# Performance work log

Hardware: AMD Instinct MI355X
Metric: run time of the kernel (lower is better)

## Reference

```python
import jax, jax.numpy as jnp
import numpy as np

S, B, D, T, E, H = 8, 32, 5, 30, 768, 128


def _time_lstm(Wall, ball, Uall, bU, Wd, bd, x, ts):
    # x: [N,T,E], ts: [N,T]. Faithful to torch TimeLSTM: c_tmp uses sigmoid,
    # and the returned per-step 'outputs' are the o-gates (as in the source).
    N = x.shape[0]
    h0 = jnp.zeros((N, Wd.shape[0]), x.dtype)

    def step(carry, inp):
        h, c = carry
        xt, tt = inp
        c_s1 = jnp.tanh(c @ Wd + bd)
        c_adj = c - c_s1 + c_s1 * tt[:, None]
        g = jax.nn.sigmoid(h @ Wall + ball + xt @ Uall + bU)
        f, i, o, ct = jnp.split(g, 4, axis=1)
        c2 = f * c_adj + i * ct
        h2 = o * jnp.tanh(c2)
        return (h2, c2), o

    _, outs = jax.lax.scan(step, (h0, h0), (x.swapaxes(0, 1), ts.swapaxes(0, 1)))
    return outs.swapaxes(0, 1)  # [N,T,H]


def _attn(W1, b1, W2, b2, V, bV, full, last, lens):
    # full: [N,T,H]; last: [N,H] or [N,1,H]
    s1 = last @ W1 + b1
    if s1.ndim == 2:
        s1 = s1[:, None, :]
    score = jnp.tanh(s1 + full @ W2 + b2) @ V + bV  # [N,T,1]
    if lens is not None:
        mask = jnp.arange(full.shape[1])[None, :] < lens[:, None]
        score = jnp.where(mask[..., None], score, -jnp.inf)
    w = jax.nn.softmax(score, axis=1)
    return jnp.sum(w * full, axis=1)  # [N,H]


def _lstm(Wih, bih, Whh, bhh, x):
    # standard torch LSTM gate order i,f,g,o; x: [N,D,H]
    N = x.shape[0]
    Hh = Whh.shape[0]
    h0 = jnp.zeros((N, Hh), x.dtype)

    def step(carry, xt):
        h, c = carry
        g = xt @ Wih + bih + h @ Whh + bhh
        i, f, gg, o = jnp.split(g, 4, axis=1)
        c2 = jax.nn.sigmoid(f) * c + jax.nn.sigmoid(i) * jnp.tanh(gg)
        h2 = jax.nn.sigmoid(o) * jnp.tanh(c2)
        return (h2, c2), h2

    (h, c), hs = jax.lax.scan(step, (h0, h0), x.swapaxes(0, 1))
    return hs.swapaxes(0, 1), h  # [N,D,H], [N,H]


def _per_stock(tl_Wall, tl_ball, tl_Uall, tl_bU, tl_Wd, tl_bd,
               a1_W1, a1_b1, a1_W2, a1_b2, a1_V, a1_bV,
               l2_Wih, l2_bih, l2_Whh, l2_bhh,
               a2_W1, a2_b1, a2_W2, a2_b2, a2_V, a2_bV,
               x1_W, x1_b, x2_W, x2_b, sent, lens, times):
    # sent: [B,D,T,E], lens: [B,D] int, times: [B,D,T]
    b, d, t, e = sent.shape
    x = sent.reshape(b * d, t, e)
    ts = times.reshape(b * d, t)
    ln = lens.reshape(b * d)
    outs = _time_lstm(tl_Wall, tl_ball, tl_Uall, tl_bU, tl_Wd, tl_bd, x, ts)
    idx = jnp.clip(ln - 1, 0, t - 1)
    hn = outs[jnp.arange(b * d), idx]
    hn = jnp.where((ln > 0)[:, None], hn, 0.0)
    ctx = _attn(a1_W1, a1_b1, a1_W2, a1_b2, a1_V, a1_bV, outs, hn, ln)  # [B*D,H]
    seq = ctx.reshape(b, d, -1)
    hs, hlast = _lstm(l2_Wih, l2_bih, l2_Whh, l2_bhh, seq)
    ctx2 = _attn(a2_W1, a2_b1, a2_W2, a2_b2, a2_V, a2_bV, hs, hlast[:, None, :], None)
    y = jax.nn.relu(ctx2 @ x1_W + x1_b)  # dropout is eval-mode identity
    return y @ x2_W + x2_b  # [B,64]


def setup_inputs() -> dict:
    key = jax.random.key(0)
    ks = iter(jax.random.split(key, 64))

    def p(*shape):
        return jax.random.normal(next(ks), shape, jnp.float32) * 0.05

    H4 = 4 * H
    return {
        'stock_feats': jax.random.normal(next(ks), (B, 2 * S + 1), jnp.float32),
        'sentence_feat': jax.random.normal(next(ks), (B, S, D, T, E), jnp.float32),
        'time_feats': jax.random.uniform(next(ks), (B, S, D, T), jnp.float32),
        'len_tweets': jax.random.randint(next(ks), (B, S, D), 1, T + 1),
        'tl_Wall': p(S, H, H4), 'tl_ball': p(S, H4),
        'tl_Uall': p(S, E, H4), 'tl_bU': p(S, H4),
        'tl_Wd': p(S, H, H), 'tl_bd': p(S, H),
        'a1_W1': p(S, H, H), 'a1_b1': p(S, H), 'a1_W2': p(S, H, H), 'a1_b2': p(S, H),
        'a1_V': p(S, H, 1), 'a1_bV': p(S, 1),
        'l2_Wih': p(S, H, H4), 'l2_bih': p(S, H4), 'l2_Whh': p(S, H, H4), 'l2_bhh': p(S, H4),
        'a2_W1': p(S, H, H), 'a2_b1': p(S, H), 'a2_W2': p(S, H, H), 'a2_b2': p(S, H),
        'a2_V': p(S, H, 1), 'a2_bV': p(S, 1),
        'x1_W': p(S, H, H), 'x1_b': p(S, H), 'x2_W': p(S, H, 64), 'x2_b': p(S, 64),
        'h1_W': p(2 * S + 1, 64), 'h1_b': p(64),
        'h2_W': p(64, 32), 'h2_b': p(32),
        'hc_W': p(64 * S + 32, S), 'hc_b': p(S),
    }


def reference(stock_feats, sentence_feat, time_feats, len_tweets,
              tl_Wall, tl_ball, tl_Uall, tl_bU, tl_Wd, tl_bd,
              a1_W1, a1_b1, a1_W2, a1_b2, a1_V, a1_bV,
              l2_Wih, l2_bih, l2_Whh, l2_bhh,
              a2_W1, a2_b1, a2_W2, a2_b2, a2_V, a2_bV,
              x1_W, x1_b, x2_W, x2_b,
              h1_W, h1_b, h2_W, h2_b, hc_W, hc_b):
    sent = sentence_feat.transpose(1, 0, 2, 3, 4)  # [S,B,D,T,E]
    lens = len_tweets.transpose(1, 0, 2)           # [S,B,D]
    times = time_feats.transpose(1, 0, 2, 3)       # [S,B,D,T]
    per = jax.vmap(_per_stock)(
        tl_Wall, tl_ball, tl_Uall, tl_bU, tl_Wd, tl_bd,
        a1_W1, a1_b1, a1_W2, a1_b2, a1_V, a1_bV,
        l2_Wih, l2_bih, l2_Whh, l2_bhh,
        a2_W1, a2_b1, a2_W2, a2_b2, a2_V, a2_bV,
        x1_W, x1_b, x2_W, x2_b, sent, lens, times)  # [S,B,64]
    text = per.transpose(1, 0, 2).reshape(sent.shape[1], -1)  # [B, S*64]
    xs = jax.nn.relu(stock_feats @ h1_W + h1_b) @ h2_W + h2_b  # [B,32]
    full = jnp.concatenate([xs, text], axis=1)
    return jnp.tanh(full @ hc_W + hc_b)  # [B,S]
```

## Files before the change

kernel.cpp:

```cpp
#include <hip/hip_runtime.h>
#include <cstddef>


typedef __attribute__((ext_vector_type(8))) _Float16 f16x8;
typedef __attribute__((ext_vector_type(4))) _Float16 f16x4;
typedef __attribute__((ext_vector_type(2))) _Float16 f16x2;
typedef __attribute__((ext_vector_type(4))) float f32x4;

__device__ __forceinline__ float rcp_(float x) { return __builtin_amdgcn_rcpf(x); }
__device__ __forceinline__ float sigf(float x) { return rcp_(1.0f + __expf(-x)); }
__device__ __forceinline__ float tanhf_(float x) { return 1.0f - 2.0f * rcp_(__expf(2.0f * x) + 1.0f); }

__device__ __forceinline__ void barrier_lds_only() {
  asm volatile("s_waitcnt lgkmcnt(0)" ::: "memory");
  __builtin_amdgcn_s_barrier();
  __builtin_amdgcn_sched_barrier(0);
}

__global__ __launch_bounds__(256) void k0_rowmap(const int* __restrict__ lens,
                                                 int* __restrict__ rowmap,
                                                 int* __restrict__ Ms) {
  const int s = blockIdx.x;
  const int tid = threadIdx.x;
  __shared__ int st[160];
  __shared__ int ln[160];
  if (tid < 160) {
    const int b = tid / 5, d = tid % 5;
    ln[tid] = lens[(b * 8 + s) * 5 + d];
  }
  __syncthreads();
  if (tid == 0) {
    int run = 0;
    for (int n = 0; n < 160; ++n) { st[n] = run; run += ln[n]; }
    Ms[s] = run;
  }
  __syncthreads();
  if (tid < 160) {
    const int base = st[tid], l = ln[tid];
    for (int t = 0; t < l; ++t) rowmap[s * 4800 + base + t] = tid * 30 + t;
  }
}

__global__ __launch_bounds__(256) void k0_usplit(const float* __restrict__ U,
                                                 _Float16* __restrict__ Uh) {
  const int s = blockIdx.z;
  const int k0 = blockIdx.x * 64;
  const int n0 = blockIdx.y * 64;
  const int tid = threadIdx.x;
  __shared__ _Float16 Th[64 * 66];
  const float* Us = U + (size_t)s * 768 * 512;
#pragma unroll
  for (int rep = 0; rep < 16; ++rep) {
    const int idx = rep * 256 + tid;
    const int r = idx >> 6, c = idx & 63;
    Th[r * 66 + c] = (_Float16)Us[(size_t)(k0 + r) * 512 + n0 + c];
  }
  __syncthreads();
  _Float16* uhs = Uh + (size_t)s * 512 * 768;
#pragma unroll
  for (int rep = 0; rep < 8; ++rep) {
    const int idx = rep * 256 + tid;
    const int nn = idx >> 5;
    const int kp = (idx & 31) * 2;
    const f16x2 h2 = {Th[kp * 66 + nn], Th[(kp + 1) * 66 + nn]};
    *(f16x2*)&uhs[(size_t)(n0 + nn) * 768 + k0 + kp] = h2;
  }
}

__global__ __launch_bounds__(256) void k0_wprep(const float* __restrict__ Wall,
                                                const float* __restrict__ Wd,
                                                _Float16* __restrict__ Wfh,
                                                _Float16* __restrict__ Dfh) {
  const int w = blockIdx.x, s = blockIdx.y;
  const int tid = threadIdx.x;
  const float* Ws = Wall + (size_t)s * 65536;
  _Float16* oh = Wfh + (size_t)(s * 8 + w) * 8192;
  for (int c = tid; c < 1024; c += 256) {
    const int kt = c >> 8, nt = (c >> 6) & 3, l = c & 63;
    const int n = nt * 128 + w * 16 + (l & 15);
    const int kb = kt * 32 + ((l >> 4) << 3);
    f16x8 hv;
#pragma unroll
    for (int e = 0; e < 8; ++e) hv[e] = (_Float16)Ws[(size_t)(kb + e) * 512 + n];
    *(f16x8*)&oh[c * 8] = hv;
  }
  {
    const float* Ds = Wd + (size_t)s * 16384;
    _Float16* od = Dfh + (size_t)(s * 8 + w) * 2048;
    const int c = tid;
    const int kt = c >> 6, l = c & 63;
    const int n = w * 16 + (l & 15);
    const int kb = kt * 32 + ((l >> 4) << 3);
    f16x8 hv;
#pragma unroll
    for (int e = 0; e < 8; ++e) hv[e] = (_Float16)Ds[(size_t)(kb + e) * 128 + n];
    *(f16x8*)&od[c * 8] = hv;
  }
}

__global__ __launch_bounds__(256) void k0_aprep(const float* __restrict__ W1,
                                                const float* __restrict__ W2,
                                                _Float16* __restrict__ W1f,
                                                _Float16* __restrict__ W2f) {
  const int w = blockIdx.x, s = blockIdx.y;
  const int c = threadIdx.x;
  const int kt = c >> 6, l = c & 63;
  const int n = w * 16 + (l & 15);
  const int kb = kt * 32 + ((l >> 4) << 3);
  const float* W1s = W1 + (size_t)s * 16384;
  const float* W2s = W2 + (size_t)s * 16384;
  f16x8 v1, v2;
#pragma unroll
  for (int e = 0; e < 8; ++e) {
    v1[e] = (_Float16)W1s[(size_t)(kb + e) * 128 + n];
    v2[e] = (_Float16)W2s[(size_t)(kb + e) * 128 + n];
  }
  *(f16x8*)&W1f[(size_t)(s * 8 + w) * 2048 + c * 8] = v1;
  *(f16x8*)&W2f[(size_t)(s * 8 + w) * 2048 + c * 8] = v2;
}

__global__ __launch_bounds__(256, 4) void k1_xu(const float* __restrict__ sent,
                                                const _Float16* __restrict__ Uh,
                                                const float* __restrict__ bU,
                                                const int* __restrict__ rowmap,
                                                const int* __restrict__ Ms,
                                                float* __restrict__ XU) {
  const int s = blockIdx.x;
  const int M = Ms[s];
  const int nt = blockIdx.y & 3;
  const int mt = blockIdx.y >> 2;
  if (mt * 128 >= M) return;
  const int tid = threadIdx.x;
  const int lane = tid & 63, wid = tid >> 6;
  const int wm = wid >> 1, wn = wid & 1;

  __shared__ _Float16 Al[2][128 * 32];
  __shared__ _Float16 Bh[2][128 * 32];

  const int ar1 = tid >> 2;
  const int chk = tid & 3;
  const int afk = chk * 8;
  const int fw = (ar1 ^ (ar1 >> 2)) & 3;
  const int wA1 = ar1 * 32 + ((chk ^ fw) * 8);
  const int wA2 = wA1 + 64 * 32;

  const int* rms = rowmap + s * 4800;
  const float* asrc1;
  const float* asrc2;
  {
    int i1 = mt * 128 + ar1; if (i1 > M - 1) i1 = M - 1;
    const int grow = rms[i1];
    const int nn = grow / 30, tt = grow % 30, ab = nn / 5, ad = nn % 5;
    asrc1 = sent + (size_t)((((ab * 8 + s) * 5 + ad) * 30) + tt) * 768 + afk;
  }
  {
    int i2 = mt * 128 + ar1 + 64; if (i2 > M - 1) i2 = M - 1;
    const int grow = rms[i2];
    const int nn = grow / 30, tt = grow % 30, ab = nn / 5, ad = nn % 5;
    asrc2 = sent + (size_t)((((ab * 8 + s) * 5 + ad) * 30) + tt) * 768 + afk;
  }
  const _Float16* UhS = Uh + (size_t)s * 512 * 768;
  const _Float16* bh1 = UhS + (size_t)(nt * 128 + ar1) * 768 + afk;
  const _Float16* bh2 = UhS + (size_t)(nt * 128 + ar1 + 64) * 768 + afk;

  const int q = lane >> 4;
  const int l15 = lane & 15;
  int aoff[4], boff[4];
#pragma unroll
  for (int f = 0; f < 4; ++f) {
    {
      const int row = wm * 64 + f * 16 + l15;
      const int fr = (row ^ (row >> 2)) & 3;
      aoff[f] = row * 32 + ((q ^ fr) * 8);
    }
    {
      const int row = wn * 64 + f * 16 + l15;
      const int fr = (row ^ (row >> 2)) & 3;
      boff[f] = row * 32 + ((q ^ fr) * 8);
    }
  }

  f32x4 acc[4][4];
#pragma unroll
  for (int i = 0; i < 4; ++i)
#pragma unroll
    for (int j = 0; j < 4; ++j) acc[i][j] = (f32x4){0.f, 0.f, 0.f, 0.f};

  {
    const float4 a1a = *(const float4*)(asrc1);
    const float4 a1b = *(const float4*)(asrc1 + 4);
    const float4 a2a = *(const float4*)(asrc2);
    const float4 a2b = *(const float4*)(asrc2 + 4);
    const f16x8 vh1 = *(const f16x8*)(bh1);
    const f16x8 vh2 = *(const f16x8*)(bh2);
    f16x8 h1, h2;
    h1[0]=(_Float16)a1a.x; h1[1]=(_Float16)a1a.y; h1[2]=(_Float16)a1a.z; h1[3]=(_Float16)a1a.w;
    h1[4]=(_Float16)a1b.x; h1[5]=(_Float16)a1b.y; h1[6]=(_Float16)a1b.z; h1[7]=(_Float16)a1b.w;
    h2[0]=(_Float16)a2a.x; h2[1]=(_Float16)a2a.y; h2[2]=(_Float16)a2a.z; h2[3]=(_Float16)a2a.w;
    h2[4]=(_Float16)a2b.x; h2[5]=(_Float16)a2b.y; h2[6]=(_Float16)a2b.z; h2[7]=(_Float16)a2b.w;
    *(f16x8*)&Al[0][wA1] = h1;
    *(f16x8*)&Al[0][wA2] = h2;
    *(f16x8*)&Bh[0][wA1] = vh1;
    *(f16x8*)&Bh[0][wA2] = vh2;
  }
  __syncthreads();

  int cur = 0;
  for (int ks = 0; ks < 24; ++ks) {
    const int nxt = cur ^ 1;
    const bool more = (ks < 23);
    float4 a1a, a1b, a2a, a2b;
    f16x8 vh1, vh2;
    if (more) {
      const int ko = (ks + 1) * 32;
      a1a = *(const float4*)(asrc1 + ko);
      a1b = *(const float4*)(asrc1 + ko + 4);
      a2a = *(const float4*)(asrc2 + ko);
      a2b = *(const float4*)(asrc2 + ko + 4);
      vh1 = *(const f16x8*)(bh1 + ko);
      vh2 = *(const f16x8*)(bh2 + ko);
    }
    {
      const _Float16* Ab = &Al[cur][0];
      const _Float16* Bhb = &Bh[cur][0];
      f16x8 af[4], bhf[4];
#pragma unroll
      for (int fm = 0; fm < 4; ++fm) af[fm] = *(const f16x8*)&Ab[aoff[fm]];
#pragma unroll
      for (int fn = 0; fn < 4; ++fn) bhf[fn] = *(const f16x8*)&Bh[cur][0 + boff[fn]];
#pragma unroll
      for (int fm = 0; fm < 4; ++fm)
#pragma unroll
        for (int fn = 0; fn < 4; ++fn)
          acc[fm][fn] = __builtin_amdgcn_mfma_f32_16x16x32_f16(af[fm], bhf[fn], acc[fm][fn], 0, 0, 0);
    }
    if (more) {
      f16x8 h1, h2;
      h1[0]=(_Float16)a1a.x; h1[1]=(_Float16)a1a.y; h1[2]=(_Float16)a1a.z; h1[3]=(_Float16)a1a.w;
      h1[4]=(_Float16)a1b.x; h1[5]=(_Float16)a1b.y; h1[6]=(_Float16)a1b.z; h1[7]=(_Float16)a1b.w;
      h2[0]=(_Float16)a2a.x; h2[1]=(_Float16)a2a.y; h2[2]=(_Float16)a2a.z; h2[3]=(_Float16)a2a.w;
      h2[4]=(_Float16)a2b.x; h2[5]=(_Float16)a2b.y; h2[6]=(_Float16)a2b.z; h2[7]=(_Float16)a2b.w;
      *(f16x8*)&Al[nxt][wA1] = h1;
      *(f16x8*)&Al[nxt][wA2] = h2;
      *(f16x8*)&Bh[nxt][wA1] = vh1;
      *(f16x8*)&Bh[nxt][wA2] = vh2;
    }
    barrier_lds_only();
    cur = nxt;
  }

  const int lq = lane >> 4;
  const int colbase = nt * 128 + wn * 64;
  const int ibase = mt * 128 + wm * 64;
  float* XUs = XU + (size_t)s * 4800 * 512;
  int rowm[4][4];
#pragma unroll
  for (int fm = 0; fm < 4; ++fm)
#pragma unroll
    for (int r = 0; r < 4; ++r) {
      const int i = ibase + fm * 16 + lq * 4 + r;
      rowm[fm][r] = (i < M) ? rms[i] : -1;
    }
#pragma unroll
  for (int fn = 0; fn < 4; ++fn) {
    const int col = colbase + fn * 16 + l15;
    const float bias = bU[s * 512 + col];
#pragma unroll
    for (int fm = 0; fm < 4; ++fm)
#pragma unroll
      for (int r = 0; r < 4; ++r) {
        const int row = rowm[fm][r];
        if (row >= 0) XUs[(size_t)row * 512 + col] = acc[fm][fn][r] + bias;
      }
  }
}

__global__ __launch_bounds__(512, 2) void k2_tlstm(const _Float16* __restrict__ Wfh,
                                                   const _Float16* __restrict__ Dfh,
                                                   const float* __restrict__ ball,
                                                   const float* __restrict__ bd,
                                                   const float* __restrict__ XU,
                                                   const float* __restrict__ times,
                                                   const int* __restrict__ lens,
                                                   float* __restrict__ outs,
                                                   float* __restrict__ hn) {
  const int s = blockIdx.x;
  const int mg = blockIdx.y;
  const int tid = threadIdx.x;
  const int w = tid >> 6, l = tid & 63;

  __shared__ _Float16 hhb[2][2048];
  __shared__ _Float16 chb[2][2048];
  __shared__ float xut[2][16 * 516];
  __shared__ float tsh[16 * 32];
  __shared__ int lensh[16];

  if (tid < 16) {
    const int n = mg * 16 + tid;
    lensh[tid] = lens[((n / 5) * 8 + s) * 5 + (n % 5)];
  }
  if (tid < 480) {
    const int r = tid / 30, c = tid % 30;
    const int n = mg * 16 + r;
    tsh[r * 32 + c] = times[(((n / 5) * 8 + s) * 5 + (n % 5)) * 30 + c];
  }

  f16x8 Bh[16], Dh[4];
  {
    const _Float16* wb = Wfh + (size_t)(s * 8 + w) * 8192 + l * 8;
    const _Float16* db = Dfh + (size_t)(s * 8 + w) * 2048 + l * 8;
#pragma unroll
    for (int c = 0; c < 16; ++c) Bh[c] = *(const f16x8*)&wb[c * 512];
#pragma unroll
    for (int c = 0; c < 4; ++c) Dh[c] = *(const f16x8*)&db[c * 512];
  }

  const int hd = w * 16 + (l & 15);
  const int rq0 = (l >> 4) * 4;
  const int lp0 = rq0 | (((hd >> 3) & 3) << 4);
  const int eoff0 = ((hd >> 5) * 64 + lp0) * 8 + (hd & 7);

#pragma unroll
  for (int q = 0; q < 4; ++q) {
    hhb[0][eoff0 + q * 8] = (_Float16)0.f;
    chb[0][eoff0 + q * 8] = (_Float16)0.f;
  }

  int n_q[4];
#pragma unroll
  for (int q = 0; q < 4; ++q) n_q[q] = mg * 16 + rq0 + q;
  float blr[4];
#pragma unroll
  for (int g = 0; g < 4; ++g) blr[g] = ball[s * 512 + g * 128 + hd];
  const float bdj = bd[s * 128 + hd];

  const int sr = tid >> 5;
  const int sc = tid & 31;
  const float* xsrc = XU + (size_t)(s * 160 + mg * 16 + sr) * 30 * 512 + sc * 4;
  const int xdst = sr * 516 + sc * 4;

  __syncthreads();

  int len_q[4];
  int maxlen = 0;
#pragma unroll
  for (int i = 0; i < 16; ++i) maxlen = max(maxlen, lensh[i]);
#pragma unroll
  for (int q = 0; q < 4; ++q) len_q[q] = lensh[rq0 + q];

  float creg[4] = {0.f, 0.f, 0.f, 0.f};
  float hreg[4] = {0.f, 0.f, 0.f, 0.f};
  float oprev[4] = {0.f, 0.f, 0.f, 0.f};

  {
    float4 v0 = *(const float4*)(xsrc);
    float4 v1 = *(const float4*)(xsrc + 128);
    float4 v2 = *(const float4*)(xsrc + 256);
    float4 v3 = *(const float4*)(xsrc + 384);
    *(float4*)&xut[0][xdst]       = v0;
    *(float4*)&xut[0][xdst + 128] = v1;
    *(float4*)&xut[0][xdst + 256] = v2;
    *(float4*)&xut[0][xdst + 384] = v3;
  }
  __syncthreads();

  for (int t = 0; t < maxlen; ++t) {
    const int p = t & 1;

    if (t > 0) {
      const int tp = t - 1;
#pragma unroll
      for (int q = 0; q < 4; ++q) {
        if (tp < len_q[q]) {
          outs[((size_t)(s * 160 + n_q[q]) * 30 + tp) * 128 + hd] = oprev[q];
          if (tp == len_q[q] - 1) hn[(size_t)(s * 160 + n_q[q]) * 128 + hd] = oprev[q];
        }
      }
    }

    float4 pv0, pv1, pv2, pv3;
    const bool more = (t + 1 < maxlen);
    if (more) {
      const float* xp = xsrc + (size_t)(t + 1) * 512;
      pv0 = *(const float4*)(xp);
      pv1 = *(const float4*)(xp + 128);
      pv2 = *(const float4*)(xp + 256);
      pv3 = *(const float4*)(xp + 384);
    }

    f32x4 amA[4], amB[4], dm;
#pragma unroll
    for (int g = 0; g < 4; ++g) {
      amA[g] = (f32x4){0.f, 0.f, 0.f, 0.f};
      amB[g] = (f32x4){0.f, 0.f, 0.f, 0.f};
    }
    dm = (f32x4){0.f, 0.f, 0.f, 0.f};
#pragma unroll
    for (int kt = 0; kt < 2; ++kt) {
      const f16x8 ah0 = *(const f16x8*)&hhb[p][(kt * 64 + l) * 8];
      const f16x8 ah1 = *(const f16x8*)&hhb[p][((kt + 2) * 64 + l) * 8];
      const f16x8 cf0 = *(const f16x8*)&chb[p][(kt * 64 + l) * 8];
      const f16x8 cf1 = *(const f16x8*)&chb[p][((kt + 2) * 64 + l) * 8];
#pragma unroll
      for (int g = 0; g < 4; ++g) {
        amA[g] = __builtin_amdgcn_mfma_f32_16x16x32_f16(ah0, Bh[kt * 4 + g], amA[g], 0, 0, 0);
        amB[g] = __builtin_amdgcn_mfma_f32_16x16x32_f16(ah1, Bh[(kt + 2) * 4 + g], amB[g], 0, 0, 0);
      }
      dm = __builtin_amdgcn_mfma_f32_16x16x32_f16(cf0, Dh[kt], dm, 0, 0, 0);
      dm = __builtin_amdgcn_mfma_f32_16x16x32_f16(cf1, Dh[kt + 2], dm, 0, 0, 0);
    }

#pragma unroll
    for (int q = 0; q < 4; ++q) {
      if (t < len_q[q]) {
        const float* xr = &xut[p][(rq0 + q) * 516 + hd];
        const float tt = tsh[(rq0 + q) * 32 + t];
        const float cs1 = tanhf_(dm[q] + bdj);
        const float f  = sigf(amA[0][q] + amB[0][q] + xr[0]   + blr[0]);
        const float ii = sigf(amA[1][q] + amB[1][q] + xr[128] + blr[1]);
        const float o  = sigf(amA[2][q] + amB[2][q] + xr[256] + blr[2]);
        const float ct = sigf(amA[3][q] + amB[3][q] + xr[384] + blr[3]);
        const float c2 = f * (creg[q] + cs1 * (tt - 1.f)) + ii * ct;
        creg[q] = c2;
        hreg[q] = o * tanhf_(c2);
        oprev[q] = o;
      }
      hhb[p ^ 1][eoff0 + q * 8] = (_Float16)hreg[q];
      chb[p ^ 1][eoff0 + q * 8] = (_Float16)creg[q];
    }

    if (more) {
      *(float4*)&xut[p ^ 1][xdst]       = pv0;
      *(float4*)&xut[p ^ 1][xdst + 128] = pv1;
      *(float4*)&xut[p ^ 1][xdst + 256] = pv2;
      *(float4*)&xut[p ^ 1][xdst + 384] = pv3;
    }
    barrier_lds_only();
  }

  {
    const int tp = maxlen - 1;
#pragma unroll
    for (int q = 0; q < 4; ++q) {
      if (tp >= 0 && tp < len_q[q]) {
        outs[((size_t)(s * 160 + n_q[q]) * 30 + tp) * 128 + hd] = oprev[q];
        if (tp == len_q[q] - 1) hn[(size_t)(s * 160 + n_q[q]) * 128 + hd] = oprev[q];
      }
    }
  }
}

__global__ __launch_bounds__(512, 2) void k3_attn1(const _Float16* __restrict__ W1f,
                                                   const _Float16* __restrict__ W2f,
                                                   const float* __restrict__ b1,
                                                   const float* __restrict__ b2,
                                                   const float* __restrict__ V,
                                                   const float* __restrict__ outs,
                                                   const float* __restrict__ hn,
                                                   const int* __restrict__ lens,
                                                   float* __restrict__ ctx) {
  const int s = blockIdx.x;
  const int sg = blockIdx.y;
  const int tid = threadIdx.x;
  const int w = tid >> 6, l = tid & 63;
  const int nbase = s * 160 + sg * 8;

  __shared__ _Float16 osh[32768];
  __shared__ float u[16][132];
  __shared__ float red[8][8][32];
  __shared__ float score[8][32];
  __shared__ int lensh[8];

  if (tid < 8) {
    const int n = sg * 8 + tid;
    lensh[tid] = lens[((n / 5) * 8 + s) * 5 + (n % 5)];
  }

#pragma unroll
  for (int i = 0; i < 8; ++i) {
    const int c = tid + i * 512;
    const int nl = c >> 9;
    const int th = (c >> 8) & 1;
    const int kt = (c >> 6) & 3;
    const int lp = c & 63;
    const int t15 = lp & 15;
    const int kb = kt * 32 + (lp >> 4) * 8;
    const int t = th * 16 + t15;
    f16x8 v;
    if (t < 30) {
      const float* src = outs + ((size_t)(nbase + nl) * 30 + t) * 128 + kb;
      const float4 a = *(const float4*)(src);
      const float4 b = *(const float4*)(src + 4);
      v[0]=(_Float16)a.x; v[1]=(_Float16)a.y; v[2]=(_Float16)a.z; v[3]=(_Float16)a.w;
      v[4]=(_Float16)b.x; v[5]=(_Float16)b.y; v[6]=(_Float16)b.z; v[7]=(_Float16)b.w;
    } else {
      v = (f16x8){(_Float16)0.f,(_Float16)0.f,(_Float16)0.f,(_Float16)0.f,
                  (_Float16)0.f,(_Float16)0.f,(_Float16)0.f,(_Float16)0.f};
    }
    *(f16x8*)&osh[c * 8] = v;
  }

  f16x8 W1r[4], W2r[4];
  {
    const _Float16* w1b = W1f + (size_t)(s * 8 + w) * 2048 + l * 8;
    const _Float16* w2b = W2f + (size_t)(s * 8 + w) * 2048 + l * 8;
#pragma unroll
    for (int kt = 0; kt < 4; ++kt) {
      W1r[kt] = *(const f16x8*)&w1b[kt * 512];
      W2r[kt] = *(const f16x8*)&w2b[kt * 512];
    }
  }

  const int hd = w * 16 + (l & 15);
  const float Vhd = V[s * 128 + hd];
  const float b12 = b1[s * 128 + hd] + b2[s * 128 + hd];
  const int kc = (l >> 4) << 3;

  {
    const int rsrc = min(l & 15, 7);
    f32x4 dm = (f32x4){0.f, 0.f, 0.f, 0.f};
#pragma unroll
    for (int kt = 0; kt < 4; ++kt) {
      const float* hp = hn + (size_t)(nbase + rsrc) * 128 + kt * 32 + kc;
      const float4 a = *(const float4*)(hp);
      const float4 b = *(const float4*)(hp + 4);
      f16x8 ah;
      ah[0]=(_Float16)a.x; ah[1]=(_Float16)a.y; ah[2]=(_Float16)a.z; ah[3]=(_Float16)a.w;
      ah[4]=(_Float16)b.x; ah[5]=(_Float16)b.y; ah[6]=(_Float16)b.z; ah[7]=(_Float16)b.w;
      dm = __builtin_amdgcn_mfma_f32_16x16x32_f16(ah, W1r[kt], dm, 0, 0, 0);
    }
#pragma unroll
    for (int q = 0; q < 4; ++q) u[(l >> 4) * 4 + q][hd] = dm[q] + b12;
  }
  __syncthreads();

#pragma unroll
  for (int m = 0; m < 16; ++m) {
    const int nl = m >> 1, th = m & 1;
    const int cbase = ((nl * 2 + th) * 4) * 64;
    f32x4 acc = (f32x4){0.f, 0.f, 0.f, 0.f};
#pragma unroll
    for (int kt = 0; kt < 4; ++kt) {
      const f16x8 ah = *(const f16x8*)&osh[(cbase + kt * 64 + l) * 8];
      acc = __builtin_amdgcn_mfma_f32_16x16x32_f16(ah, W2r[kt], acc, 0, 0, 0);
    }
    const float uv = u[nl][hd];
#pragma unroll
    for (int q = 0; q < 4; ++q) {
      float p = tanhf_(acc[q] + uv) * Vhd;
      p += __shfl_xor(p, 1);
      p += __shfl_xor(p, 2);
      p += __shfl_xor(p, 4);
      p += __shfl_xor(p, 8);
      const int t = th * 16 + (l >> 4) * 4 + q;
      if ((l & 15) == 0 && t < 30) red[w][nl][t] = p;
    }
  }
  __syncthreads();

  if (tid < 256) {
    const int nl = tid >> 5, t = tid & 31;
    if (t < 30) {
      float sc = 0.f;
#pragma unroll
      for (int ww = 0; ww < 8; ++ww) sc += red[ww][nl][t];
      score[nl][t] = sc;
    }
  }
  __syncthreads();

  {
    const int nl = tid >> 6, jg = tid & 63;
    const int len = lensh[nl];
    float mx = -1e30f;
    for (int t = 0; t < len; ++t) mx = fmaxf(mx, score[nl][t]);
    const float* ob = outs + (size_t)(nbase + nl) * 30 * 128 + jg * 2;
    float sum = 0.f;
    float cx0 = 0.f, cx1 = 0.f;
    for (int t = 0; t < len; ++t) {
      const float e = __expf(score[nl][t] - mx);
      sum += e;
      const float2 o2 = *(const float2*)(ob + (size_t)t * 128);
      cx0 += e * o2.x; cx1 += e * o2.y;
    }
    const float r = rcp_(sum);
    float2 res = {cx0 * r, cx1 * r};
    *(float2*)&ctx[(size_t)(nbase + nl) * 128 + jg * 2] = res;
  }
}

__global__ __launch_bounds__(512, 2) void k4_lstm2(const float* __restrict__ Wih,
                                                   const float* __restrict__ bih,
                                                   const float* __restrict__ Whh,
                                                   const float* __restrict__ bhh,
                                                   const float* __restrict__ ctx,
                                                   float* __restrict__ hsout,
                                                   float* __restrict__ hlast) {
  const int s = blockIdx.y, b = blockIdx.x;
  const int gj = threadIdx.x;
  __shared__ float xs[5][128];
  __shared__ float hsm[128];
  __shared__ float gsh[512];

  for (int idx = gj; idx < 640; idx += 512)
    (&xs[0][0])[idx] = ctx[(size_t)(s * 160 + b * 5) * 128 + idx];
  if (gj < 128) hsm[gj] = 0.f;
  __syncthreads();

  const float* Wis = Wih + (size_t)s * 65536;
  const float* Whs = Whh + (size_t)s * 65536;
  const float bias = bih[s * 512 + gj] + bhh[s * 512 + gj];
  float xw[5] = {bias, bias, bias, bias, bias};
  float whh[128];
#pragma unroll
  for (int k = 0; k < 128; ++k) {
    const float wi = Wis[k * 512 + gj];
    whh[k] = Whs[k * 512 + gj];
#pragma unroll
    for (int dd = 0; dd < 5; ++dd) xw[dd] += xs[dd][k] * wi;
  }

  float c = 0.f;
  for (int dd = 0; dd < 5; ++dd) {
    float g = xw[dd];
#pragma unroll
    for (int k = 0; k < 128; ++k) g += hsm[k] * whh[k];
    gsh[gj] = g;
    __syncthreads();
    if (gj < 128) {
      const int j = gj;
      const float c2 = sigf(gsh[128 + j]) * c + sigf(gsh[j]) * tanhf_(gsh[256 + j]);
      const float h2 = sigf(gsh[384 + j]) * tanhf_(c2);
      c = c2;
      hsm[j] = h2;
      hsout[((size_t)(s * 32 + b) * 5 + dd) * 128 + j] = h2;
      if (dd == 4) hlast[(size_t)(s * 32 + b) * 128 + j] = h2;
    }
    __syncthreads();
  }
}

__global__ __launch_bounds__(128) void k5_attn2(const float* __restrict__ W1,
                                                const float* __restrict__ b1,
                                                const float* __restrict__ W2,
                                                const float* __restrict__ b2,
                                                const float* __restrict__ V,
                                                const float* __restrict__ bV,
                                                const float* __restrict__ x1W,
                                                const float* __restrict__ x1b,
                                                const float* __restrict__ x2W,
                                                const float* __restrict__ x2b,
                                                const float* __restrict__ hs,
                                                const float* __restrict__ hlast,
                                                float* __restrict__ y) {
  const int s = blockIdx.y, b = blockIdx.x, j = threadIdx.x;
  __shared__ float hl[128], hsm[5][128], t1[128], cs2[128], sc[5], red[2];
  hl[j] = hlast[(size_t)(s * 32 + b) * 128 + j];
  const float* hsrc = hs + (size_t)(s * 32 + b) * 640;
  for (int idx = j; idx < 640; idx += 128) (&hsm[0][0])[idx] = hsrc[idx];
  __syncthreads();

  const float* W1s = W1 + (size_t)s * 16384;
  const float* W2s = W2 + (size_t)s * 16384;
  float u = b1[s * 128 + j] + b2[s * 128 + j];
  for (int k = 0; k < 128; ++k) u += hl[k] * W1s[k * 128 + j];
  const float Vj = V[s * 128 + j];
  const int lane = j & 63, wid = j >> 6;

  for (int d = 0; d < 5; ++d) {
    float a = u;
    for (int k = 0; k < 128; ++k) a += hsm[d][k] * W2s[k * 128 + j];
    float p = tanhf_(a) * Vj;
#pragma unroll
    for (int off = 32; off; off >>= 1) p += __shfl_down(p, off);
    if (lane == 0) red[wid] = p;
    __syncthreads();
    if (j == 0) sc[d] = red[0] + red[1] + bV[s];
    __syncthreads();
  }

  float m = -1e30f;
  for (int d = 0; d < 5; ++d) m = fmaxf(m, sc[d]);
  float sum = 0.f;
  for (int d = 0; d < 5; ++d) sum += __expf(sc[d] - m);
  float cx = 0.f;
  for (int d = 0; d < 5; ++d) cx += __expf(sc[d] - m) * hsm[d][j];
  cs2[j] = cx / sum;
  __syncthreads();

  float a = x1b[s * 128 + j];
  for (int k = 0; k < 128; ++k) a += cs2[k] * x1W[(size_t)s * 16384 + k * 128 + j];
  t1[j] = fmaxf(a, 0.f);
  __syncthreads();

  if (j < 64) {
    float yy = x2b[s * 64 + j];
    for (int k = 0; k < 128; ++k) yy += t1[k] * x2W[(size_t)(s * 128 + k) * 64 + j];
    y[(size_t)(s * 32 + b) * 64 + j] = yy;
  }
}

__global__ __launch_bounds__(256) void k6_final(const float* __restrict__ stock,
                                                const float* __restrict__ h1W,
                                                const float* __restrict__ h1b,
                                                const float* __restrict__ h2W,
                                                const float* __restrict__ h2b,
                                                const float* __restrict__ hcW,
                                                const float* __restrict__ hcb,
                                                const float* __restrict__ yws,
                                                float* __restrict__ out) {
  const int tid = threadIdx.x;
  __shared__ float sf[32 * 17];
  __shared__ float hid[32 * 64];
  __shared__ float xs[32 * 32];
  for (int idx = tid; idx < 544; idx += 256) sf[idx] = stock[idx];
  __syncthreads();
  for (int idx = tid; idx < 2048; idx += 256) {
    const int b = idx >> 6, k = idx & 63;
    float a = h1b[k];
    for (int q = 0; q < 17; ++q) a += sf[b * 17 + q] * h1W[q * 64 + k];
    hid[idx] = fmaxf(a, 0.f);
  }
  __syncthreads();
  for (int idx = tid; idx < 1024; idx += 256) {
    const int b = idx >> 5, mm = idx & 31;
    float a = h2b[mm];
    for (int k = 0; k < 64; ++k) a += hid[b * 64 + k] * h2W[k * 32 + mm];
    xs[idx] = a;
  }
  __syncthreads();
  {
    const int b = tid >> 3, o = tid & 7;
    float a = hcb[o];
    for (int c = 0; c < 32; ++c) a += xs[b * 32 + c] * hcW[c * 8 + o];
    for (int c = 32; c < 544; ++c) {
      const int ss = (c - 32) >> 6, k = (c - 32) & 63;
      a += yws[((size_t)ss * 32 + b) * 64 + k] * hcW[c * 8 + o];
    }
    out[tid] = tanhf_(a);
  }
}

extern "C" void kernel_launch(void* const* d_in, const int* in_sizes, int n_in,
                              void* d_out, int out_size, void* d_ws, size_t ws_size,
                              hipStream_t stream) {
  (void)in_sizes; (void)n_in; (void)out_size; (void)ws_size;
  const float* stock = (const float*)d_in[0];
  const float* sent  = (const float*)d_in[1];
  const float* times = (const float*)d_in[2];
  const int*   lens  = (const int*)d_in[3];
  const float* tlWall = (const float*)d_in[4];
  const float* tlball = (const float*)d_in[5];
  const float* tlUall = (const float*)d_in[6];
  const float* tlbU   = (const float*)d_in[7];
  const float* tlWd   = (const float*)d_in[8];
  const float* tlbd   = (const float*)d_in[9];
  const float* a1W1 = (const float*)d_in[10];
  const float* a1b1 = (const float*)d_in[11];
  const float* a1W2 = (const float*)d_in[12];
  const float* a1b2 = (const float*)d_in[13];
  const float* a1V  = (const float*)d_in[14];
  const float* a1bV = (const float*)d_in[15];
  const float* l2Wih = (const float*)d_in[16];
  const float* l2bih = (const float*)d_in[17];
  const float* l2Whh = (const float*)d_in[18];
  const float* l2bhh = (const float*)d_in[19];
  const float* a2W1 = (const float*)d_in[20];
  const float* a2b1 = (const float*)d_in[21];
  const float* a2W2 = (const float*)d_in[22];
  const float* a2b2 = (const float*)d_in[23];
  const float* a2V  = (const float*)d_in[24];
  const float* a2bV = (const float*)d_in[25];
  const float* x1W  = (const float*)d_in[26];
  const float* x1b  = (const float*)d_in[27];
  const float* x2W  = (const float*)d_in[28];
  const float* x2b  = (const float*)d_in[29];
  const float* h1W  = (const float*)d_in[30];
  const float* h1b  = (const float*)d_in[31];
  const float* h2W  = (const float*)d_in[32];
  const float* h2b  = (const float*)d_in[33];
  const float* hcW  = (const float*)d_in[34];
  const float* hcb  = (const float*)d_in[35];

  float* ws = (float*)d_ws;
  float* XU    = ws;
  float* outs  = XU + 19660800;
  float* hnb   = outs + 4915200;
  float* ctx   = hnb + 163840;
  float* hsb   = ctx + 163840;
  float* hlast = hsb + 163840;
  float* yb    = hlast + 32768;
  _Float16* Uhw = (_Float16*)(yb + 16384);
  _Float16* Wfh = Uhw + 8 * 512 * 768;
  _Float16* Dfh = Wfh + 8 * 8 * 8192;
  _Float16* W1f = Dfh + 8 * 8 * 2048;
  _Float16* W2f = W1f + 8 * 8 * 2048;
  int* rowmap = (int*)(W2f + 8 * 8 * 2048);
  int* Msd    = rowmap + 8 * 4800;

  k0_rowmap<<<8, 256, 0, stream>>>(lens, rowmap, Msd);
  k0_usplit<<<dim3(12, 8, 8), 256, 0, stream>>>(tlUall, Uhw);
  k0_wprep<<<dim3(8, 8), 256, 0, stream>>>(tlWall, tlWd, Wfh, Dfh);
  k0_aprep<<<dim3(8, 8), 256, 0, stream>>>(a1W1, a1W2, W1f, W2f);
  k1_xu<<<dim3(8, 152), 256, 0, stream>>>(sent, Uhw, tlbU, rowmap, Msd, XU);
  k2_tlstm<<<dim3(8, 10), 512, 0, stream>>>(Wfh, Dfh, tlball, tlbd, XU, times, lens, outs, hnb);
  k3_attn1<<<dim3(8, 20), 512, 0, stream>>>(W1f, W2f, a1b1, a1b2, a1V, outs, hnb, lens, ctx);
  k4_lstm2<<<dim3(32, 8), 512, 0, stream>>>(l2Wih, l2bih, l2Whh, l2bhh, ctx, hsb, hlast);
  k5_attn2<<<dim3(32, 8), 128, 0, stream>>>(a2W1, a2b1, a2W2, a2b2, a2V, a2bV, x1W, x1b, x2W, x2b, hsb, hlast, yb);
  k6_final<<<1, 256, 0, stream>>>(stock, h1W, h1b, h2W, h2b, hcW, hcb, yb, (float*)d_out);
}
```

Before: 210.3 us.

## Process two row groups per TimeLSTM block and read XU directly from global

The TimeLSTM recurrence kernel now handles two 16-row groups per block, halving the grid from 80 to 40 blocks. The two groups are interleaved in each step, so their MFMA chains can hide each other's latency. The LDS staging of the XU gate inputs is removed; each thread loads its gate inputs from global memory at the start of every step, with no prefetch. The aim is to reuse the register-resident weights across more rows and give each wave more independent work. The cost is fewer active CUs and global-load latency exposed on the serial critical path of every timestep.

```diff
diff --git a/kernel.cpp b/kernel.cpp
--- a/kernel.cpp
+++ b/kernel.cpp
@@ -227,7 +227,7 @@
 #pragma unroll
       for (int fm = 0; fm < 4; ++fm) af[fm] = *(const f16x8*)&Ab[aoff[fm]];
 #pragma unroll
-      for (int fn = 0; fn < 4; ++fn) bhf[fn] = *(const f16x8*)&Bh[cur][0 + boff[fn]];
+      for (int fn = 0; fn < 4; ++fn) bhf[fn] = *(const f16x8*)&Bhb[boff[fn]];
 #pragma unroll
       for (int fm = 0; fm < 4; ++fm)
 #pragma unroll
@@ -285,24 +285,25 @@
                                                    float* __restrict__ outs,
                                                    float* __restrict__ hn) {
   const int s = blockIdx.x;
-  const int mg = blockIdx.y;
+  const int pg = blockIdx.y;
   const int tid = threadIdx.x;
   const int w = tid >> 6, l = tid & 63;
 
-  __shared__ _Float16 hhb[2][2048];
-  __shared__ _Float16 chb[2][2048];
-  __shared__ float xut[2][16 * 516];
-  __shared__ float tsh[16 * 32];
-  __shared__ int lensh[16];
-
-  if (tid < 16) {
-    const int n = mg * 16 + tid;
-    lensh[tid] = lens[((n / 5) * 8 + s) * 5 + (n % 5)];
-  }
-  if (tid < 480) {
-    const int r = tid / 30, c = tid % 30;
-    const int n = mg * 16 + r;
-    tsh[r * 32 + c] = times[(((n / 5) * 8 + s) * 5 + (n % 5)) * 30 + c];
+  __shared__ _Float16 hhb[2][2][2048];
+  __shared__ _Float16 chb[2][2][2048];
+  __shared__ float tsh[2][16 * 32];
+  __shared__ int lensh[2][16];
+
+  if (tid < 32) {
+    const int gi = tid >> 4, r = tid & 15;
+    const int n = (pg * 2 + gi) * 16 + r;
+    lensh[gi][r] = lens[((n / 5) * 8 + s) * 5 + (n % 5)];
+  }
+  for (int idx = tid; idx < 960; idx += 512) {
+    const int gi = idx / 480;
+    const int rr = (idx % 480) / 30, cc = idx % 30;
+    const int n = (pg * 2 + gi) * 16 + rr;
+    tsh[gi][rr * 32 + cc] = times[(((n / 5) * 8 + s) * 5 + (n % 5)) * 30 + cc];
   }
 
   f16x8 Bh[16], Dh[4];
@@ -321,48 +322,43 @@
   const int eoff0 = ((hd >> 5) * 64 + lp0) * 8 + (hd & 7);
 
 #pragma unroll
-  for (int q = 0; q < 4; ++q) {
-    hhb[0][eoff0 + q * 8] = (_Float16)0.f;
-    chb[0][eoff0 + q * 8] = (_Float16)0.f;
-  }
-
-  int n_q[4];
-#pragma unroll
-  for (int q = 0; q < 4; ++q) n_q[q] = mg * 16 + rq0 + q;
+  for (int gi = 0; gi < 2; ++gi)
+#pragma unroll
+    for (int qq = 0; qq < 4; ++qq) {
+      hhb[gi][0][eoff0 + qq * 8] = (_Float16)0.f;
+      chb[gi][0][eoff0 + qq * 8] = (_Float16)0.f;
+    }
+
+  int n_q[2][4];
+  size_t xub[2][4];
+#pragma unroll
+  for (int gi = 0; gi < 2; ++gi)
+#pragma unroll
+    for (int qq = 0; qq < 4; ++qq) {
+      n_q[gi][qq] = (pg * 2 + gi) * 16 + rq0 + qq;
+      xub[gi][qq] = ((size_t)(s * 160 + n_q[gi][qq])) * 30 * 512 + hd;
+    }
   float blr[4];
 #pragma unroll
   for (int g = 0; g < 4; ++g) blr[g] = ball[s * 512 + g * 128 + hd];
   const float bdj = bd[s * 128 + hd];
 
-  const int sr = tid >> 5;
-  const int sc = tid & 31;
-  const float* xsrc = XU + (size_t)(s * 160 + mg * 16 + sr) * 30 * 512 + sc * 4;
-  const int xdst = sr * 516 + sc * 4;
-
-  __syncthreads();
-
-  int len_q[4];
+  __syncthreads();
+
+  int len_q[2][4];
   int maxlen = 0;
 #pragma unroll
-  for (int i = 0; i < 16; ++i) maxlen = max(maxlen, lensh[i]);
-#pragma unroll
-  for (int q = 0; q < 4; ++q) len_q[q] = lensh[rq0 + q];
-
-  float creg[4] = {0.f, 0.f, 0.f, 0.f};
-  float hreg[4] = {0.f, 0.f, 0.f, 0.f};
-  float oprev[4] = {0.f, 0.f, 0.f, 0.f};
-
-  {
-    float4 v0 = *(const float4*)(xsrc);
-    float4 v1 = *(const float4*)(xsrc + 128);
-    float4 v2 = *(const float4*)(xsrc + 256);
-    float4 v3 = *(const float4*)(xsrc + 384);
-    *(float4*)&xut[0][xdst]       = v0;
-    *(float4*)&xut[0][xdst + 128] = v1;
-    *(float4*)&xut[0][xdst + 256] = v2;
-    *(float4*)&xut[0][xdst + 384] = v3;
-  }
-  __syncthreads();
+  for (int gi = 0; gi < 2; ++gi)
+#pragma unroll
+    for (int i = 0; i < 16; ++i) maxlen = max(maxlen, lensh[gi][i]);
+#pragma unroll
+  for (int gi = 0; gi < 2; ++gi)
+#pragma unroll
+    for (int qq = 0; qq < 4; ++qq) len_q[gi][qq] = lensh[gi][rq0 + qq];
+
+  float creg[2][4] = {};
+  float hreg[2][4] = {};
+  float oprev[2][4] = {};
 
   for (int t = 0; t < maxlen; ++t) {
     const int p = t & 1;
@@ -370,83 +366,88 @@
     if (t > 0) {
       const int tp = t - 1;
 #pragma unroll
-      for (int q = 0; q < 4; ++q) {
-        if (tp < len_q[q]) {
-          outs[((size_t)(s * 160 + n_q[q]) * 30 + tp) * 128 + hd] = oprev[q];
-          if (tp == len_q[q] - 1) hn[(size_t)(s * 160 + n_q[q]) * 128 + hd] = oprev[q];
+      for (int gi = 0; gi < 2; ++gi)
+#pragma unroll
+        for (int qq = 0; qq < 4; ++qq) {
+          if (tp < len_q[gi][qq]) {
+            outs[((size_t)(s * 160 + n_q[gi][qq]) * 30 + tp) * 128 + hd] = oprev[gi][qq];
+            if (tp == len_q[gi][qq] - 1)
+              hn[(size_t)(s * 160 + n_q[gi][qq]) * 128 + hd] = oprev[gi][qq];
+          }
+        }
+    }
+
+    float xg[2][4][4];
+#pragma unroll
+    for (int gi = 0; gi < 2; ++gi)
+#pragma unroll
+      for (int qq = 0; qq < 4; ++qq) {
+        const float* xp = XU + xub[gi][qq] + (size_t)t * 512;
+#pragma unroll
+        for (int g = 0; g < 4; ++g) xg[gi][qq][g] = xp[g * 128];
+      }
+
+    f32x4 amA[2][4], amB[2][4], dm[2];
+#pragma unroll
+    for (int gi = 0; gi < 2; ++gi) {
+#pragma unroll
+      for (int g = 0; g < 4; ++g) {
+        amA[gi][g] = (f32x4){0.f, 0.f, 0.f, 0.f};
+        amB[gi][g] = (f32x4){0.f, 0.f, 0.f, 0.f};
+      }
+      dm[gi] = (f32x4){0.f, 0.f, 0.f, 0.f};
+#pragma unroll
+      for (int kt = 0; kt < 2; ++kt) {
+        const f16x8 ah0 = *(const f16x8*)&hhb[gi][p][(kt * 64 + l) * 8];
+        const f16x8 ah1 = *(const f16x8*)&hhb[gi][p][((kt + 2) * 64 + l) * 8];
+        const f16x8 cf0 = *(const f16x8*)&chb[gi][p][(kt * 64 + l) * 8];
+        const f16x8 cf1 = *(const f16x8*)&chb[gi][p][((kt + 2) * 64 + l) * 8];
+#pragma unroll
+        for (int g = 0; g < 4; ++g) {
+          amA[gi][g] = __builtin_amdgcn_mfma_f32_16x16x32_f16(ah0, Bh[kt * 4 + g], amA[gi][g], 0, 0, 0);
+          amB[gi][g] = __builtin_amdgcn_mfma_f32_16x16x32_f16(ah1, Bh[(kt + 2) * 4 + g], amB[gi][g], 0, 0, 0);
+        }
+        dm[gi] = __builtin_amdgcn_mfma_f32_16x16x32_f16(cf0, Dh[kt], dm[gi], 0, 0, 0);
+        dm[gi] = __builtin_amdgcn_mfma_f32_16x16x32_f16(cf1, Dh[kt + 2], dm[gi], 0, 0, 0);
+      }
+    }
+
+#pragma unroll
+    for (int gi = 0; gi < 2; ++gi) {
+#pragma unroll
+      for (int qq = 0; qq < 4; ++qq) {
+        if (t < len_q[gi][qq]) {
+          const float tt = tsh[gi][(rq0 + qq) * 32 + t];
+          const float cs1 = tanhf_(dm[gi][qq] + bdj);
+          const float f  = sigf(amA[gi][0][qq] + amB[gi][0][qq] + xg[gi][qq][0] + blr[0]);
+          const float ii = sigf(amA[gi][1][qq] + amB[gi][1][qq] + xg[gi][qq][1] + blr[1]);
+          const float o  = sigf(amA[gi][2][qq] + amB[gi][2][qq] + xg[gi][qq][2] + blr[2]);
+          const float ct = sigf(amA[gi][3][qq] + amB[gi][3][qq] + xg[gi][qq][3] + blr[3]);
+          const float c2 = f * (creg[gi][qq] + cs1 * (tt - 1.f)) + ii * ct;
+          creg[gi][qq] = c2;
+          hreg[gi][qq] = o * tanhf_(c2);
+          oprev[gi][qq] = o;
+        }
+        hhb[gi][p ^ 1][eoff0 + qq * 8] = (_Float16)hreg[gi][qq];
+        chb[gi][p ^ 1][eoff0 + qq * 8] = (_Float16)creg[gi][qq];
+      }
+    }
+
+    barrier_lds_only();
+  }
+
+  {
+    const int tp = maxlen - 1;
+#pragma unroll
+    for (int gi = 0; gi < 2; ++gi)
+#pragma unroll
+      for (int qq = 0; qq < 4; ++qq) {
+        if (tp >= 0 && tp < len_q[gi][qq]) {
+          outs[((size_t)(s * 160 + n_q[gi][qq]) * 30 + tp) * 128 + hd] = oprev[gi][qq];
+          if (tp == len_q[gi][qq] - 1)
+            hn[(size_t)(s * 160 + n_q[gi][qq]) * 128 + hd] = oprev[gi][qq];
         }
       }
-    }
-
-    float4 pv0, pv1, pv2, pv3;
-    const bool more = (t + 1 < maxlen);
-    if (more) {
-      const float* xp = xsrc + (size_t)(t + 1) * 512;
-      pv0 = *(const float4*)(xp);
-      pv1 = *(const float4*)(xp + 128);
-      pv2 = *(const float4*)(xp + 256);
-      pv3 = *(const float4*)(xp + 384);
-    }
-
-    f32x4 amA[4], amB[4], dm;
-#pragma unroll
-    for (int g = 0; g < 4; ++g) {
-      amA[g] = (f32x4){0.f, 0.f, 0.f, 0.f};
-      amB[g] = (f32x4){0.f, 0.f, 0.f, 0.f};
-    }
-    dm = (f32x4){0.f, 0.f, 0.f, 0.f};
-#pragma unroll
-    for (int kt = 0; kt < 2; ++kt) {
-      const f16x8 ah0 = *(const f16x8*)&hhb[p][(kt * 64 + l) * 8];
-      const f16x8 ah1 = *(const f16x8*)&hhb[p][((kt + 2) * 64 + l) * 8];
-      const f16x8 cf0 = *(const f16x8*)&chb[p][(kt * 64 + l) * 8];
-      const f16x8 cf1 = *(const f16x8*)&chb[p][((kt + 2) * 64 + l) * 8];
-#pragma unroll
-      for (int g = 0; g < 4; ++g) {
-        amA[g] = __builtin_amdgcn_mfma_f32_16x16x32_f16(ah0, Bh[kt * 4 + g], amA[g], 0, 0, 0);
-        amB[g] = __builtin_amdgcn_mfma_f32_16x16x32_f16(ah1, Bh[(kt + 2) * 4 + g], amB[g], 0, 0, 0);
-      }
-      dm = __builtin_amdgcn_mfma_f32_16x16x32_f16(cf0, Dh[kt], dm, 0, 0, 0);
-      dm = __builtin_amdgcn_mfma_f32_16x16x32_f16(cf1, Dh[kt + 2], dm, 0, 0, 0);
-    }
-
-#pragma unroll
-    for (int q = 0; q < 4; ++q) {
-      if (t < len_q[q]) {
-        const float* xr = &xut[p][(rq0 + q) * 516 + hd];
-        const float tt = tsh[(rq0 + q) * 32 + t];
-        const float cs1 = tanhf_(dm[q] + bdj);
-        const float f  = sigf(amA[0][q] + amB[0][q] + xr[0]   + blr[0]);
-        const float ii = sigf(amA[1][q] + amB[1][q] + xr[128] + blr[1]);
-        const float o  = sigf(amA[2][q] + amB[2][q] + xr[256] + blr[2]);
-        const float ct = sigf(amA[3][q] + amB[3][q] + xr[384] + blr[3]);
-        const float c2 = f * (creg[q] + cs1 * (tt - 1.f)) + ii * ct;
-        creg[q] = c2;
-        hreg[q] = o * tanhf_(c2);
-        oprev[q] = o;
-      }
-      hhb[p ^ 1][eoff0 + q * 8] = (_Float16)hreg[q];
-      chb[p ^ 1][eoff0 + q * 8] = (_Float16)creg[q];
-    }
-
-    if (more) {
-      *(float4*)&xut[p ^ 1][xdst]       = pv0;
-      *(float4*)&xut[p ^ 1][xdst + 128] = pv1;
-      *(float4*)&xut[p ^ 1][xdst + 256] = pv2;
-      *(float4*)&xut[p ^ 1][xdst + 384] = pv3;
-    }
-    barrier_lds_only();
-  }
-
-  {
-    const int tp = maxlen - 1;
-#pragma unroll
-    for (int q = 0; q < 4; ++q) {
-      if (tp >= 0 && tp < len_q[q]) {
-        outs[((size_t)(s * 160 + n_q[q]) * 30 + tp) * 128 + hd] = oprev[q];
-        if (tp == len_q[q] - 1) hn[(size_t)(s * 160 + n_q[q]) * 128 + hd] = oprev[q];
-      }
-    }
   }
 }
 
@@ -803,7 +804,7 @@
   k0_wprep<<<dim3(8, 8), 256, 0, stream>>>(tlWall, tlWd, Wfh, Dfh);
   k0_aprep<<<dim3(8, 8), 256, 0, stream>>>(a1W1, a1W2, W1f, W2f);
   k1_xu<<<dim3(8, 152), 256, 0, stream>>>(sent, Uhw, tlbU, rowmap, Msd, XU);
-  k2_tlstm<<<dim3(8, 10), 512, 0, stream>>>(Wfh, Dfh, tlball, tlbd, XU, times, lens, outs, hnb);
+  k2_tlstm<<<dim3(8, 5), 512, 0, stream>>>(Wfh, Dfh, tlball, tlbd, XU, times, lens, outs, hnb);
   k3_attn1<<<dim3(8, 20), 512, 0, stream>>>(W1f, W2f, a1b1, a1b2, a1V, outs, hnb, lens, ctx);
   k4_lstm2<<<dim3(32, 8), 512, 0, stream>>>(l2Wih, l2bih, l2Whh, l2bhh, ctx, hsb, hlast);
   k5_attn2<<<dim3(32, 8), 128, 0, stream>>>(a2W1, a2b1, a2W2, a2b2, a2V, a2bV, x1W, x1b, x2W, x2b, hsb, hlast, yb);
```

New measurement: 265.7 us. 1.26x slower.
